# Kernel tuning notes

Measured on AMD Instinct MI355X. Metric: run time of the kernel, lower is better.

Reference implementation:

```python
import jax, jax.numpy as jnp
import numpy as np

B, L, C, V = 16, 600, 256, 256
OUT_SEQ = 6000
KSZ = 5
DILATIONS = (1, 2, 4)
N_BLOCKS = 10
COND = 256  # speaker(128) + noise(128)
TEMP = 10.0
EPS = 1e-5


def _ccbn(x, cond, gw, gb, bw, bb):
    # x: (B, C, L); conditional batch-norm: per-channel stats over (batch, length),
    # gamma/beta predicted from condition vector.
    mu = jnp.mean(x, axis=(0, 2), keepdims=True)
    var = jnp.var(x, axis=(0, 2), keepdims=True)
    xn = (x - mu) * jax.lax.rsqrt(var + EPS)
    gamma = 1.0 + cond @ gw + gb  # (B, C)
    beta = cond @ bw + bb         # (B, C)
    return xn * gamma[:, :, None] + beta[:, :, None]


def _conv1d(x, w, b, dil=1):
    # x: (B, C_in, L); w: (C_out, C_in, K)
    y = jax.lax.conv_general_dilated(
        x, w, window_strides=(1,), padding='SAME', rhs_dilation=(dil,),
        dimension_numbers=('NCH', 'OIH', 'NCH'))
    return y + b[None, :, None]


def setup_inputs() -> dict:
    key = jax.random.key(0)
    ks = jax.random.split(key, 20)
    s = 0.02
    inp = {
        'inputs': jax.random.randint(ks[0], (B, L), 0, V),
        'speaker_embeddings': jax.random.normal(ks[1], (B, 128), jnp.float32),
        'noise': jax.random.normal(ks[2], (B, 128), jnp.float32),
        'emb': jax.random.normal(ks[3], (V, C), jnp.float32) * s,
        # 10 blocks x 3 dilated convs
        'conv_w': jax.random.normal(ks[4], (N_BLOCKS, 3, C, C, KSZ), jnp.float32) * s,
        'conv_b': jnp.zeros((N_BLOCKS, 3, C), jnp.float32),
        # CCBN projections per conv (gamma/beta from condition)
        'g_w': jax.random.normal(ks[5], (N_BLOCKS, 3, COND, C), jnp.float32) * s,
        'g_b': jnp.zeros((N_BLOCKS, 3, C), jnp.float32),
        'b_w': jax.random.normal(ks[6], (N_BLOCKS, 3, COND, C), jnp.float32) * s,
        'b_b': jnp.zeros((N_BLOCKS, 3, C), jnp.float32),
        # TokenLength head: 2 CCBNs + conv1 (256->256,k1) + conv2 (256->1,k1)
        'tl_g_w': jax.random.normal(ks[7], (2, COND, C), jnp.float32) * s,
        'tl_g_b': jnp.zeros((2, C), jnp.float32),
        'tl_b_w': jax.random.normal(ks[8], (2, COND, C), jnp.float32) * s,
        'tl_b_b': jnp.zeros((2, C), jnp.float32),
        'tl_conv1_w': jax.random.normal(ks[9], (C, C, 1), jnp.float32) * s,
        'tl_conv1_b': jnp.zeros((C,), jnp.float32),
        'tl_conv2_w': jax.random.normal(ks[10], (1, C, 1), jnp.float32) * s,
        'tl_conv2_b': jnp.zeros((1,), jnp.float32),
    }
    return inp


def reference(inputs, speaker_embeddings, noise, emb, conv_w, conv_b,
              g_w, g_b, b_w, b_b, tl_g_w, tl_g_b, tl_b_w, tl_b_b,
              tl_conv1_w, tl_conv1_b, tl_conv2_w, tl_conv2_b):
    cond = jnp.concatenate([speaker_embeddings, noise], axis=-1)  # (B, COND)
    x = emb[inputs]                    # (B, L, C)
    x = jnp.transpose(x, (0, 2, 1))    # (B, C, L)

    # 10 unaligned blocks: residual stacks of CCBN -> ReLU -> dilated conv
    for blk in range(N_BLOCKS):
        y = x
        for j, d in enumerate(DILATIONS):
            y = jax.nn.relu(_ccbn(y, cond, g_w[blk, j], g_b[blk, j], b_w[blk, j], b_b[blk, j]))
            y = _conv1d(y, conv_w[blk, j], conv_b[blk, j], dil=d)
        x = x + y
    unaligned = x  # (B, C, L)

    # TokenLength head
    t = jax.nn.relu(_ccbn(unaligned, cond, tl_g_w[0], tl_g_b[0], tl_b_w[0], tl_b_b[0]))
    t = _conv1d(t, tl_conv1_w, tl_conv1_b)
    t = jax.nn.relu(_ccbn(t, cond, tl_g_w[1], tl_g_b[1], tl_b_w[1], tl_b_b[1]))
    t = _conv1d(t, tl_conv2_w, tl_conv2_b)  # (B, 1, L)
    token_lengths = jax.nn.relu(t[:, 0, :])  # (B, L)

    token_ends = jnp.cumsum(token_lengths, axis=-1)        # (B, L)
    token_centers = token_ends - token_lengths / 2.0        # (B, L)
    aligned_lengths = token_ends

    out_pos = jnp.arange(OUT_SEQ, dtype=jnp.float32)         # (OUT,)
    diff = token_centers[:, None, :] - out_pos[None, :, None]  # (B, OUT, L)
    logits = -(diff * diff) / TEMP
    weights = jax.nn.softmax(logits, axis=-1)                # (B, OUT, L)

    feats = jnp.transpose(unaligned, (0, 2, 1))              # (B, L, C)
    aligned_features = jnp.einsum('bol,blc->boc', weights, feats)  # (B, OUT, C)
    return aligned_features, aligned_lengths
```

## Files before the change

kernel.cpp:

```cpp
#include <hip/hip_runtime.h>
#include <math.h>

#define EPSv 1e-5f

typedef short short8 __attribute__((ext_vector_type(8)));
typedef float floatx4 __attribute__((ext_vector_type(4)));

__device__ __forceinline__ unsigned short f2bf(float x) {
  unsigned u = __float_as_uint(x);
  unsigned r = (u + 0x7fffu + ((u >> 16) & 1u)) >> 16;
  return (unsigned short)r;
}

__global__ void k_zero(float* __restrict__ p) {
  p[blockIdx.x * 256 + threadIdx.x] = 0.f;
}

__global__ void k_gamma_beta(const float* __restrict__ spk, const float* __restrict__ noise,
                             const float* __restrict__ g_w, const float* __restrict__ g_b,
                             const float* __restrict__ b_w, const float* __restrict__ b_b,
                             const float* __restrict__ tl_g_w, const float* __restrict__ tl_g_b,
                             const float* __restrict__ tl_b_w, const float* __restrict__ tl_b_b,
                             float* __restrict__ gammas, float* __restrict__ betas) {
  __shared__ float condl[16*256];
  int t = threadIdx.x;
  for (int idx = t; idx < 4096; idx += 256) {
    int b = idx >> 8, k = idx & 255;
    condl[idx] = (k < 128) ? spk[b*128 + k] : noise[b*128 + k - 128];
  }
  __syncthreads();
  int i = blockIdx.x;
  const float *gw, *bw, *gbias, *bbias;
  if (i < 30) { gw = g_w + (size_t)i*65536; bw = b_w + (size_t)i*65536; gbias = g_b + i*256; bbias = b_b + i*256; }
  else { int j = i - 30; gw = tl_g_w + (size_t)j*65536; bw = tl_b_w + (size_t)j*65536; gbias = tl_g_b + j*256; bbias = tl_b_b + j*256; }
  int co = (t & 63) + blockIdx.y * 64;
  int slot = t >> 6;
  float g[4] = {0.f,0.f,0.f,0.f}, bt[4] = {0.f,0.f,0.f,0.f};
  for (int k = 0; k < 256; ++k) {
    float gwv = gw[k*256 + co];
    float bwv = bw[k*256 + co];
    #pragma unroll
    for (int bb = 0; bb < 4; ++bb) {
      float cv = condl[(slot*4 + bb)*256 + k];
      g[bb]  = fmaf(cv, gwv, g[bb]);
      bt[bb] = fmaf(cv, bwv, bt[bb]);
    }
  }
  #pragma unroll
  for (int bb = 0; bb < 4; ++bb) {
    int b = slot*4 + bb;
    gammas[i*4096 + b*256 + co] = 1.0f + g[bb] + gbias[co];
    betas [i*4096 + b*256 + co] = bt[bb] + bbias[co];
  }
}

template<int TAPS>
__device__ __forceinline__ void wprep_body(const float* __restrict__ src,
                                           unsigned short* __restrict__ dst,
                                           int cotile, int chunk, int t) {
  int cow = t >> 2, ci8 = (t & 3) * 8;
  const float* s0 = src + ((size_t)(cotile*64 + cow)*256 + chunk*32 + ci8)*TAPS;
  float v[8*TAPS];
  #pragma unroll
  for (int i = 0; i < 8*TAPS; ++i) v[i] = s0[i];
  unsigned short* dblk = dst + (size_t)cotile*(8*TAPS*4096) + (size_t)chunk*(TAPS*4096);
  #pragma unroll
  for (int tap = 0; tap < TAPS; ++tap) {
    unsigned hi2[4], lo2[4];
    #pragma unroll
    for (int jj = 0; jj < 4; ++jj) {
      float a = v[(jj*2+0)*TAPS + tap], b = v[(jj*2+1)*TAPS + tap];
      unsigned short ha = f2bf(a), hb = f2bf(b);
      unsigned short la = f2bf(a - __uint_as_float((unsigned)ha << 16));
      unsigned short lb = f2bf(b - __uint_as_float((unsigned)hb << 16));
      hi2[jj] = (unsigned)ha | ((unsigned)hb << 16);
      lo2[jj] = (unsigned)la | ((unsigned)lb << 16);
    }
    uint4 H; H.x = hi2[0]; H.y = hi2[1]; H.z = hi2[2]; H.w = hi2[3];
    uint4 L; L.x = lo2[0]; L.y = lo2[1]; L.z = lo2[2]; L.w = lo2[3];
    *(uint4*)(dblk + (size_t)(tap*2)*2048 + cow*32 + ci8) = H;
    *(uint4*)(dblk + (size_t)(tap*2+1)*2048 + cow*32 + ci8) = L;
  }
}

__global__ __launch_bounds__(256) void k_wprep(const float* __restrict__ conv_w,
                                               const float* __restrict__ tl_c1_w,
                                               unsigned short* __restrict__ wp) {
  int cc = blockIdx.x;
  int cotile = blockIdx.y >> 3, chunk = blockIdx.y & 7;
  if (cc == 30) wprep_body<1>(tl_c1_w, wp + (size_t)30*655360, cotile, chunk, threadIdx.x);
  else          wprep_body<5>(conv_w + (size_t)cc*327680, wp + (size_t)cc*655360, cotile, chunk, threadIdx.x);
}

__global__ void k_embed2(const int* __restrict__ inp, const float* __restrict__ emb,
                         float* __restrict__ x, float* __restrict__ stat0) {
  int bx = blockIdx.x;
  int c = threadIdx.x;
  int r0 = bx * 60;
  float s = 0.f, s2 = 0.f;
  for (int r = 0; r < 60; ++r) {
    int row = inp[r0 + r];
    float v = emb[(size_t)row*256 + c];
    x[(size_t)(r0 + r)*256 + c] = v;
    s += v; s2 = fmaf(v, v, s2);
  }
  atomicAdd(&stat0[c], s);
  atomicAdd(&stat0[256 + c], s2);
}

template<int TAPS>
__global__ __launch_bounds__(256) void k_convm(const float* __restrict__ zin, float* __restrict__ out,
                        const float* __restrict__ stat_in, float* __restrict__ stat_out,
                        const float* __restrict__ gam, const float* __restrict__ bet,
                        const unsigned short* __restrict__ wpc,
                        const float* __restrict__ bias, int dil, int mode) {
  __shared__ unsigned short Zhi[3200];
  __shared__ unsigned short Zlo[3200];
  __shared__ float s_sc[256];
  __shared__ float s_sh[256];
  __shared__ float lsum[32];
  __shared__ float lsq[32];
  int t = threadIdx.x;
  int bx = blockIdx.x;
  int b  = bx / 10;
  int l0 = (bx % 10) * 64;
  int co0 = blockIdx.y * 32;
  int cobase = (blockIdx.y & 1) * 32;
  int PAD = ((TAPS - 1)/2) * dil;
  int ROWS = 64 + 2*PAD;
  int w = t >> 6, lane = t & 63;
  int lsub = (w & 1) * 32, cosub = (w >> 1) * 16;
  int quad = lane >> 4, nlan = lane & 15;
  if (t < 32) { lsum[t] = 0.f; lsq[t] = 0.f; }
  {
    float s = stat_in[t], s2 = stat_in[256 + t];
    float mu = s * (1.0f/9600.0f);
    float var = s2 * (1.0f/9600.0f) - mu*mu;
    float rs = rsqrtf(var + EPSv);
    float scale = rs * gam[b*256 + t];
    s_sc[t] = scale;
    s_sh[t] = fmaf(-mu, scale, bet[b*256 + t]);
  }

  floatx4 acc[2];
  acc[0] = (floatx4){0.f,0.f,0.f,0.f};
  acc[1] = (floatx4){0.f,0.f,0.f,0.f};

  const float* zb = zin + (size_t)b*600*256;
  int srow = t >> 3, fq = t & 7;
  int ar0 = (lsub + nlan) * 40 + quad * 8;
  int ar1 = (lsub + 16 + nlan) * 40 + quad * 8;

  bool va[3]; long zbase[3];
  #pragma unroll
  for (int i = 0; i < 3; ++i) {
    int r = srow + i*32;
    int gl = l0 - PAD + r;
    va[i] = (r < ROWS) && (gl >= 0) && (gl < 600);
    zbase[i] = (long)gl*256 + fq*4;
  }

  for (int chunk = 0; chunk < 8; ++chunk) {
    int ci0 = chunk * 32;
    const unsigned short* pch = wpc + (size_t)((blockIdx.y >> 1)*8 + chunk) * (TAPS*4096);
    short8 bh[TAPS], bl[TAPS];
    int cw = (cobase + cosub + nlan)*32 + quad*8;
    #pragma unroll
    for (int tap = 0; tap < TAPS; ++tap) {
      bh[tap] = *(const short8*)(pch + (size_t)(tap*2)*2048 + cw);
      bl[tap] = *(const short8*)(pch + (size_t)(tap*2+1)*2048 + cw);
    }
    float4 zr[3];
    #pragma unroll
    for (int i = 0; i < 3; ++i) {
      float4 z = {0.f,0.f,0.f,0.f};
      if (va[i]) z = *(const float4*)&zb[zbase[i] + ci0];
      zr[i] = z;
    }
    __syncthreads();
    float4 sc4 = *(const float4*)&s_sc[ci0 + fq*4];
    float4 sh4 = *(const float4*)&s_sh[ci0 + fq*4];
    #pragma unroll
    for (int i = 0; i < 3; ++i) {
      int r = srow + i*32;
      if (r < ROWS) {
        float4 z = zr[i];
        bool inr = va[i];
        float v0 = inr ? fmaxf(fmaf(z.x, sc4.x, sh4.x), 0.f) : 0.f;
        float v1 = inr ? fmaxf(fmaf(z.y, sc4.y, sh4.y), 0.f) : 0.f;
        float v2 = inr ? fmaxf(fmaf(z.z, sc4.z, sh4.z), 0.f) : 0.f;
        float v3 = inr ? fmaxf(fmaf(z.w, sc4.w, sh4.w), 0.f) : 0.f;
        unsigned short h0 = f2bf(v0), h1 = f2bf(v1), h2 = f2bf(v2), h3 = f2bf(v3);
        unsigned short e0 = f2bf(v0 - __uint_as_float((unsigned)h0 << 16));
        unsigned short e1 = f2bf(v1 - __uint_as_float((unsigned)h1 << 16));
        unsigned short e2 = f2bf(v2 - __uint_as_float((unsigned)h2 << 16));
        unsigned short e3 = f2bf(v3 - __uint_as_float((unsigned)h3 << 16));
        uint2 vh; vh.x = (unsigned)h0 | ((unsigned)h1 << 16);
        vh.y = (unsigned)h2 | ((unsigned)h3 << 16);
        uint2 vl; vl.x = (unsigned)e0 | ((unsigned)e1 << 16);
        vl.y = (unsigned)e2 | ((unsigned)e3 << 16);
        *(uint2*)&Zhi[r*40 + fq*4] = vh;
        *(uint2*)&Zlo[r*40 + fq*4] = vl;
      }
    }
    __syncthreads();
    #pragma unroll
    for (int tap = 0; tap < TAPS; ++tap) {
      int sh = tap * dil * 40;
      short8 ah0 = *(const short8*)&Zhi[ar0 + sh];
      short8 ah1 = *(const short8*)&Zhi[ar1 + sh];
      short8 al0 = *(const short8*)&Zlo[ar0 + sh];
      short8 al1 = *(const short8*)&Zlo[ar1 + sh];
      acc[0] = __builtin_amdgcn_mfma_f32_16x16x32_bf16(ah0, bh[tap], acc[0], 0, 0, 0);
      acc[0] = __builtin_amdgcn_mfma_f32_16x16x32_bf16(ah0, bl[tap], acc[0], 0, 0, 0);
      acc[0] = __builtin_amdgcn_mfma_f32_16x16x32_bf16(al0, bh[tap], acc[0], 0, 0, 0);
      acc[1] = __builtin_amdgcn_mfma_f32_16x16x32_bf16(ah1, bh[tap], acc[1], 0, 0, 0);
      acc[1] = __builtin_amdgcn_mfma_f32_16x16x32_bf16(ah1, bl[tap], acc[1], 0, 0, 0);
      acc[1] = __builtin_amdgcn_mfma_f32_16x16x32_bf16(al1, bh[tap], acc[1], 0, 0, 0);
    }
  }

  float bsv = bias[co0 + cosub + nlan];
  float ssum = 0.f, ssq = 0.f;
  #pragma unroll
  for (int mt = 0; mt < 2; ++mt) {
    #pragma unroll
    for (int r = 0; r < 4; ++r) {
      int l = l0 + lsub + mt*16 + quad*4 + r;
      if (l < 600) {
        float v = acc[mt][r] + bsv;
        float* dst = &out[((size_t)(b*600 + l))*256 + co0 + cosub + nlan];
        if (mode) v += *dst;
        *dst = v;
        ssum += v;
        ssq = fmaf(v, v, ssq);
      }
    }
  }
  ssum += __shfl_xor(ssum, 16, 64);
  ssum += __shfl_xor(ssum, 32, 64);
  ssq  += __shfl_xor(ssq, 16, 64);
  ssq  += __shfl_xor(ssq, 32, 64);
  if (quad == 0) {
    atomicAdd(&lsum[cosub + nlan], ssum);
    atomicAdd(&lsq [cosub + nlan], ssq);
  }
  __syncthreads();
  if (t < 32) {
    atomicAdd(&stat_out[co0 + t], lsum[t]);
    atomicAdd(&stat_out[256 + co0 + t], lsq[t]);
  }
}

__global__ void k_tl2(const float* __restrict__ z, const float* __restrict__ stat,
                      const float* __restrict__ gam, const float* __restrict__ bet,
                      const float* __restrict__ w2, const float* __restrict__ b2,
                      float* __restrict__ tl) {
  int t = threadIdx.x;
  int row = blockIdx.x * 4 + (t >> 6);
  int lane = t & 63;
  int b = row / 600;
  float4 s1 = *(const float4*)&stat[lane*4];
  float4 s2 = *(const float4*)&stat[256 + lane*4];
  float4 gm = *(const float4*)&gam[b*256 + lane*4];
  float4 bt = *(const float4*)&bet[b*256 + lane*4];
  float sc[4], sh[4];
  {
    float sv[4] = {s1.x, s1.y, s1.z, s1.w};
    float qv[4] = {s2.x, s2.y, s2.z, s2.w};
    float gv[4] = {gm.x, gm.y, gm.z, gm.w};
    float bv[4] = {bt.x, bt.y, bt.z, bt.w};
    #pragma unroll
    for (int i = 0; i < 4; ++i) {
      float mu = sv[i] * (1.0f/9600.0f);
      float var = qv[i] * (1.0f/9600.0f) - mu*mu;
      float rs = rsqrtf(var + EPSv);
      sc[i] = rs * gv[i];
      sh[i] = fmaf(-mu, sc[i], bv[i]);
    }
  }
  float4 zr = *(const float4*)&z[(size_t)row*256 + lane*4];
  float4 wr = *(const float4*)&w2[lane*4];
  float z0 = fmaxf(fmaf(zr.x, sc[0], sh[0]), 0.f);
  float z1 = fmaxf(fmaf(zr.y, sc[1], sh[1]), 0.f);
  float z2 = fmaxf(fmaf(zr.z, sc[2], sh[2]), 0.f);
  float z3 = fmaxf(fmaf(zr.w, sc[3], sh[3]), 0.f);
  float s = z0*wr.x + z1*wr.y + z2*wr.z + z3*wr.w;
  for (int m = 32; m >= 1; m >>= 1) s += __shfl_xor(s, m, 64);
  if (lane == 0) tl[row] = fmaxf(s + b2[0], 0.f);
}

__global__ void k_cumsum(const float* __restrict__ tl, float* __restrict__ centers,
                         float* __restrict__ out_len) {
  int b = blockIdx.x; int lane = threadIdx.x;
  float carry = 0.f;
  for (int ch = 0; ch < 10; ++ch) {
    int l = ch*64 + lane;
    float v = (l < 600) ? tl[b*600 + l] : 0.f;
    float s = v;
    #pragma unroll
    for (int off = 1; off < 64; off <<= 1) {
      float n = __shfl_up(s, off, 64);
      if (lane >= off) s += n;
    }
    float ends = carry + s;
    if (l < 600) {
      centers[b*600 + l] = ends - 0.5f*v;
      out_len[b*600 + l] = ends;
    }
    carry = __shfl(ends, 63, 64);
  }
}

__global__ void k_tobf16(const float* __restrict__ x, unsigned short* __restrict__ fbT) {
  __shared__ unsigned short T[64*66];
  int b = blockIdx.x, lt = blockIdx.y, ct = blockIdx.z;
  int t = threadIdx.x;
  int i4 = t >> 6;
  int j = t & 63;
  #pragma unroll
  for (int r = 0; r < 16; ++r) {
    int li = i4*16 + r;
    int l = lt*64 + li;
    float v = (l < 600) ? x[((size_t)(b*600 + l))*256 + ct*64 + j] : 0.f;
    T[j*66 + li] = f2bf(v);
  }
  __syncthreads();
  int row = t >> 2, seg = (t & 3) * 16;
  unsigned vv[8];
  #pragma unroll
  for (int k = 0; k < 8; ++k)
    vv[k] = *(const unsigned*)&T[row*66 + seg + k*2];
  size_t dsth = ((size_t)(b*256 + ct*64 + row))*640 + lt*64 + seg;
  unsigned* du = (unsigned*)fbT;
  uint4 a; a.x = vv[0]; a.y = vv[1]; a.z = vv[2]; a.w = vv[3];
  uint4 c4; c4.x = vv[4]; c4.y = vv[5]; c4.z = vv[6]; c4.w = vv[7];
  *(uint4*)(du + dsth/2) = a;
  *(uint4*)(du + dsth/2 + 4) = c4;
}

__global__ __launch_bounds__(256) void k_align2(const unsigned short* __restrict__ fbT,
                        const float* __restrict__ centers, float* __restrict__ outp) {
  __shared__ float cen[600];
  __shared__ float mrow[64];
  __shared__ float isum[64];
  __shared__ unsigned short Wt[64*72];
  __shared__ unsigned short Ft[256*72];
  int b = blockIdx.x;
  int o0 = blockIdx.y * 64;
  int t = threadIdx.x;
  int wv = t >> 6, lane = t & 63;
  for (int i = t; i < 600; i += 256) cen[i] = centers[b*600 + i];
  __syncthreads();
  for (int rr = 0; rr < 16; ++rr) {
    int oi = wv*16 + rr;
    float opos = (float)(o0 + oi);
    float mx = -3.0e38f;
    for (int l = lane; l < 600; l += 64) {
      float d = cen[l] - opos;
      mx = fmaxf(mx, -d*d*0.1f);
    }
    #pragma unroll
    for (int mm = 32; mm >= 1; mm >>= 1) mx = fmaxf(mx, __shfl_xor(mx, mm, 64));
    if (lane == 0) mrow[oi] = mx;
  }
  __syncthreads();
  floatx4 acc[4][4];
  #pragma unroll
  for (int i = 0; i < 4; ++i)
    #pragma unroll
    for (int j = 0; j < 4; ++j)
      acc[i][j] = (floatx4){0.f, 0.f, 0.f, 0.f};
  int quad = lane >> 4;
  int nlan = lane & 15;
  int oi_w = t >> 2;
  int sbase = t & 3;
  float mo = mrow[oi_w];
  float opos_w = (float)(o0 + oi_w);
  float psum = 0.f;
  const unsigned short* srcb = fbT + ((size_t)b*256)*640;

  for (int ch = 0; ch < 10; ++ch) {
    int lc0 = ch * 64;
    __syncthreads();
    #pragma unroll
    for (int sidx = 0; sidx < 2; ++sidx) {
      int seg = sbase + sidx*4;
      unsigned pk[4];
      #pragma unroll
      for (int jj = 0; jj < 8; jj += 2) {
        int li = lc0 + seg*8 + jj;
        float e0 = 0.f, e1 = 0.f;
        if (li < 600)     { float d = cen[li] - opos_w;     e0 = __expf(-d*d*0.1f - mo); }
        if (li + 1 < 600) { float d = cen[li + 1] - opos_w; e1 = __expf(-d*d*0.1f - mo); }
        psum += e0 + e1;
        pk[jj>>1] = (unsigned)f2bf(e0) | ((unsigned)f2bf(e1) << 16);
      }
      uint4 v; v.x = pk[0]; v.y = pk[1]; v.z = pk[2]; v.w = pk[3];
      *(uint4*)&Wt[oi_w*72 + seg*8] = v;
    }
    #pragma unroll
    for (int it = 0; it < 8; ++it) {
      int idx = t + it*256;
      int c = idx >> 3, part = idx & 7;
      uint4 v = *(const uint4*)(srcb + (size_t)c*640 + lc0 + part*8);
      *(uint4*)&Ft[c*72 + part*8] = v;
    }
    __syncthreads();
    #pragma unroll
    for (int ks = 0; ks < 2; ++ks) {
      int ko = ks*32 + quad*8;
      short8 af[4], bfr[4];
      #pragma unroll
      for (int mt = 0; mt < 4; ++mt)
        af[mt] = *(const short8*)&Wt[(mt*16 + nlan)*72 + ko];
      #pragma unroll
      for (int nt = 0; nt < 4; ++nt)
        bfr[nt] = *(const short8*)&Ft[(wv*64 + nt*16 + nlan)*72 + ko];
      #pragma unroll
      for (int mt = 0; mt < 4; ++mt)
        #pragma unroll
        for (int nt = 0; nt < 4; ++nt)
          acc[mt][nt] = __builtin_amdgcn_mfma_f32_16x16x32_bf16(af[mt], bfr[nt], acc[mt][nt], 0, 0, 0);
    }
  }
  psum += __shfl_xor(psum, 1, 64);
  psum += __shfl_xor(psum, 2, 64);
  if ((t & 3) == 0) isum[oi_w] = 1.0f / psum;
  __syncthreads();
  #pragma unroll
  for (int mt = 0; mt < 4; ++mt) {
    #pragma unroll
    for (int r = 0; r < 4; ++r) {
      int oi = mt*16 + quad*4 + r;
      int o = o0 + oi;
      if (o < 6000) {
        float sc = isum[oi];
        #pragma unroll
        for (int nt = 0; nt < 4; ++nt) {
          int c = wv*64 + nt*16 + nlan;
          outp[((size_t)b*6000 + o)*256 + c] = acc[mt][nt][r] * sc;
        }
      }
    }
  }
}

extern "C" void kernel_launch(void* const* d_in, const int* in_sizes, int n_in,
                              void* d_out, int out_size, void* d_ws, size_t ws_size,
                              hipStream_t stream) {
  const int*   inputs = (const int*)  d_in[0];
  const float* spk    = (const float*)d_in[1];
  const float* noise  = (const float*)d_in[2];
  const float* emb    = (const float*)d_in[3];
  const float* conv_w = (const float*)d_in[4];
  const float* conv_b = (const float*)d_in[5];
  const float* g_w    = (const float*)d_in[6];
  const float* g_b    = (const float*)d_in[7];
  const float* b_w    = (const float*)d_in[8];
  const float* b_b    = (const float*)d_in[9];
  const float* tl_g_w = (const float*)d_in[10];
  const float* tl_g_b = (const float*)d_in[11];
  const float* tl_b_w = (const float*)d_in[12];
  const float* tl_b_b = (const float*)d_in[13];
  const float* tl_c1_w = (const float*)d_in[14];
  const float* tl_c1_b = (const float*)d_in[15];
  const float* tl_c2_w = (const float*)d_in[16];
  const float* tl_c2_b = (const float*)d_in[17];
  float* out = (float*)d_out;

  float* ws = (float*)d_ws;
  float* x       = ws;
  float* A       = x + 2457600;
  float* Bf      = A + 2457600;
  float* gammas  = Bf + 2457600;
  float* betas   = gammas + 131072;
  float* statacc = betas + 131072;
  float* tl      = statacc + 16384;
  float* cen     = tl + 9600;
  unsigned short* wp = (unsigned short*)(cen + 9600);
  unsigned short* fbT = (unsigned short*)Bf;

  k_zero<<<dim3(64), dim3(256), 0, stream>>>(statacc);
  k_wprep<<<dim3(31, 32), dim3(256), 0, stream>>>(conv_w, tl_c1_w, wp);
  k_gamma_beta<<<dim3(32, 4), dim3(256), 0, stream>>>(spk, noise, g_w, g_b, b_w, b_b,
      tl_g_w, tl_g_b, tl_b_w, tl_b_b, gammas, betas);
  k_embed2<<<dim3(160), dim3(256), 0, stream>>>(inputs, emb, x, statacc);

  const int dils[3] = {1, 2, 4};
  for (int blk = 0; blk < 10; ++blk) {
    const float* srcs[3] = {x, A, Bf};
    float*       dsts[3] = {A, Bf, x};
    for (int j = 0; j < 3; ++j) {
      int idx = blk*3 + j;
      int mode = (j == 2) ? 1 : 0;
      k_convm<5><<<dim3(160, 8), dim3(256), 0, stream>>>(srcs[j], dsts[j],
          statacc + idx*512, statacc + (idx+1)*512,
          gammas + idx*4096, betas + idx*4096,
          wp + (size_t)idx*655360, conv_b + idx*256, dils[j], mode);
    }
  }
  k_convm<1><<<dim3(160, 8), dim3(256), 0, stream>>>(x, A,
      statacc + 30*512, statacc + 31*512,
      gammas + 30*4096, betas + 30*4096,
      wp + (size_t)30*655360, tl_c1_b, 1, 0);
  k_tl2<<<dim3(2400), dim3(256), 0, stream>>>(A, statacc + 31*512,
      gammas + 31*4096, betas + 31*4096, tl_c2_w, tl_c2_b, tl);
  k_cumsum<<<dim3(16), dim3(64), 0, stream>>>(tl, cen, out + 24576000);
  k_tobf16<<<dim3(16, 10, 4), dim3(256), 0, stream>>>(x, fbT);
  k_align2<<<dim3(16, 94), dim3(256), 0, stream>>>(fbT, cen, out);
}
```

Before: 1.662 ms.

## Precompute normalized bf16 hi/lo activations in separate kernel, load via direct-to-LDS

Moves the conditional batch-norm, ReLU and bf16 hi/lo split out of the conv kernel into a new k_norm kernel. It writes padded, chunked bf16 tiles to a workspace once per layer, so the transform is no longer repeated by all 8 output-channel blocks. The conv kernel then fills its shared-memory tiles with global_load_lds DMA transfers instead of register loads plus ALU conversion. In exchange it adds an extra kernel launch per layer and a global round trip of the normalized tensor.

```diff
diff --git a/kernel.cpp b/kernel.cpp
--- a/kernel.cpp
+++ b/kernel.cpp
@@ -1,5 +1,6 @@
 #include <hip/hip_runtime.h>
 #include <math.h>
+#include <stdint.h>
 
 #define EPSv 1e-5f
 
@@ -10,6 +11,13 @@
   unsigned u = __float_as_uint(x);
   unsigned r = (u + 0x7fffu + ((u >> 16) & 1u)) >> 16;
   return (unsigned short)r;
+}
+
+__device__ __forceinline__ void gld_lds16(const void* g, void* l) {
+  __builtin_amdgcn_global_load_lds(
+      (const __attribute__((address_space(1))) unsigned*)(uintptr_t)g,
+      (__attribute__((address_space(3))) unsigned*)(uintptr_t)l,
+      16, 0, 0);
 }
 
 __global__ void k_zero(float* __restrict__ p) {
@@ -108,16 +116,67 @@
   atomicAdd(&stat0[256 + c], s2);
 }
 
+__global__ __launch_bounds__(256) void k_norm(const float* __restrict__ z,
+                      const float* __restrict__ stat,
+                      const float* __restrict__ gam, const float* __restrict__ bet,
+                      unsigned short* __restrict__ zn) {
+  __shared__ float s_sc[32];
+  __shared__ float s_sh[32];
+  int b = blockIdx.x, chunk = blockIdx.y, rg = blockIdx.z;
+  int t = threadIdx.x;
+  if (t < 32) {
+    int c = chunk*32 + t;
+    float s = stat[c], s2 = stat[256 + c];
+    float mu = s * (1.0f/9600.0f);
+    float var = s2 * (1.0f/9600.0f) - mu*mu;
+    float rs = rsqrtf(var + EPSv);
+    float scale = rs * gam[b*256 + c];
+    s_sc[t] = scale;
+    s_sh[t] = fmaf(-mu, scale, bet[b*256 + c]);
+  }
+  __syncthreads();
+  int srow = t >> 3, fq = t & 7;
+  float4 sc4 = *(const float4*)&s_sc[fq*4];
+  float4 sh4 = *(const float4*)&s_sh[fq*4];
+  unsigned short* zh = zn + ((size_t)b*8 + chunk)*54400 + fq*4;
+  unsigned short* zl = zh + 27200;
+  const float* zb = z + (size_t)b*600*256 + chunk*32 + fq*4;
+  #pragma unroll
+  for (int i = 0; i < 4; ++i) {
+    int r = rg*128 + i*32 + srow;
+    if (r < 680) {
+      int l = r - 8;
+      uint2 vh; vh.x = 0u; vh.y = 0u;
+      uint2 vl; vl.x = 0u; vl.y = 0u;
+      if (l >= 0 && l < 600) {
+        float4 zv = *(const float4*)&zb[(size_t)l*256];
+        float v0 = fmaxf(fmaf(zv.x, sc4.x, sh4.x), 0.f);
+        float v1 = fmaxf(fmaf(zv.y, sc4.y, sh4.y), 0.f);
+        float v2 = fmaxf(fmaf(zv.z, sc4.z, sh4.z), 0.f);
+        float v3 = fmaxf(fmaf(zv.w, sc4.w, sh4.w), 0.f);
+        unsigned short h0 = f2bf(v0), h1 = f2bf(v1), h2 = f2bf(v2), h3 = f2bf(v3);
+        unsigned short e0 = f2bf(v0 - __uint_as_float((unsigned)h0 << 16));
+        unsigned short e1 = f2bf(v1 - __uint_as_float((unsigned)h1 << 16));
+        unsigned short e2 = f2bf(v2 - __uint_as_float((unsigned)h2 << 16));
+        unsigned short e3 = f2bf(v3 - __uint_as_float((unsigned)h3 << 16));
+        vh.x = (unsigned)h0 | ((unsigned)h1 << 16);
+        vh.y = (unsigned)h2 | ((unsigned)h3 << 16);
+        vl.x = (unsigned)e0 | ((unsigned)e1 << 16);
+        vl.y = (unsigned)e2 | ((unsigned)e3 << 16);
+      }
+      *(uint2*)&zh[(size_t)r*40] = vh;
+      *(uint2*)&zl[(size_t)r*40] = vl;
+    }
+  }
+}
+
 template<int TAPS>
-__global__ __launch_bounds__(256) void k_convm(const float* __restrict__ zin, float* __restrict__ out,
-                        const float* __restrict__ stat_in, float* __restrict__ stat_out,
-                        const float* __restrict__ gam, const float* __restrict__ bet,
+__global__ __launch_bounds__(256) void k_convm(const unsigned short* __restrict__ zn,
+                        float* __restrict__ out, float* __restrict__ stat_out,
                         const unsigned short* __restrict__ wpc,
                         const float* __restrict__ bias, int dil, int mode) {
-  __shared__ unsigned short Zhi[3200];
-  __shared__ unsigned short Zlo[3200];
-  __shared__ float s_sc[256];
-  __shared__ float s_sh[256];
+  __shared__ __align__(16) unsigned short Zhi[3584];
+  __shared__ __align__(16) unsigned short Zlo[3584];
   __shared__ float lsum[32];
   __shared__ float lsq[32];
   int t = threadIdx.x;
@@ -127,41 +186,21 @@
   int co0 = blockIdx.y * 32;
   int cobase = (blockIdx.y & 1) * 32;
   int PAD = ((TAPS - 1)/2) * dil;
-  int ROWS = 64 + 2*PAD;
   int w = t >> 6, lane = t & 63;
   int lsub = (w & 1) * 32, cosub = (w >> 1) * 16;
   int quad = lane >> 4, nlan = lane & 15;
   if (t < 32) { lsum[t] = 0.f; lsq[t] = 0.f; }
-  {
-    float s = stat_in[t], s2 = stat_in[256 + t];
-    float mu = s * (1.0f/9600.0f);
-    float var = s2 * (1.0f/9600.0f) - mu*mu;
-    float rs = rsqrtf(var + EPSv);
-    float scale = rs * gam[b*256 + t];
-    s_sc[t] = scale;
-    s_sh[t] = fmaf(-mu, scale, bet[b*256 + t]);
-  }
 
   floatx4 acc[2];
   acc[0] = (floatx4){0.f,0.f,0.f,0.f};
   acc[1] = (floatx4){0.f,0.f,0.f,0.f};
 
-  const float* zb = zin + (size_t)b*600*256;
-  int srow = t >> 3, fq = t & 7;
+  const unsigned short* zbase = zn + (size_t)b*435200 + (size_t)(l0 - PAD + 8)*40 + (size_t)lane*8;
   int ar0 = (lsub + nlan) * 40 + quad * 8;
-  int ar1 = (lsub + 16 + nlan) * 40 + quad * 8;
-
-  bool va[3]; long zbase[3];
-  #pragma unroll
-  for (int i = 0; i < 3; ++i) {
-    int r = srow + i*32;
-    int gl = l0 - PAD + r;
-    va[i] = (r < ROWS) && (gl >= 0) && (gl < 600);
-    zbase[i] = (long)gl*256 + fq*4;
-  }
+  int ar1 = ar0 + 640;
 
   for (int chunk = 0; chunk < 8; ++chunk) {
-    int ci0 = chunk * 32;
+    __syncthreads();
     const unsigned short* pch = wpc + (size_t)((blockIdx.y >> 1)*8 + chunk) * (TAPS*4096);
     short8 bh[TAPS], bl[TAPS];
     int cw = (cobase + cosub + nlan)*32 + quad*8;
@@ -170,38 +209,13 @@
       bh[tap] = *(const short8*)(pch + (size_t)(tap*2)*2048 + cw);
       bl[tap] = *(const short8*)(pch + (size_t)(tap*2+1)*2048 + cw);
     }
-    float4 zr[3];
-    #pragma unroll
-    for (int i = 0; i < 3; ++i) {
-      float4 z = {0.f,0.f,0.f,0.f};
-      if (va[i]) z = *(const float4*)&zb[zbase[i] + ci0];
-      zr[i] = z;
-    }
-    __syncthreads();
-    float4 sc4 = *(const float4*)&s_sc[ci0 + fq*4];
-    float4 sh4 = *(const float4*)&s_sh[ci0 + fq*4];
-    #pragma unroll
-    for (int i = 0; i < 3; ++i) {
-      int r = srow + i*32;
-      if (r < ROWS) {
-        float4 z = zr[i];
-        bool inr = va[i];
-        float v0 = inr ? fmaxf(fmaf(z.x, sc4.x, sh4.x), 0.f) : 0.f;
-        float v1 = inr ? fmaxf(fmaf(z.y, sc4.y, sh4.y), 0.f) : 0.f;
-        float v2 = inr ? fmaxf(fmaf(z.z, sc4.z, sh4.z), 0.f) : 0.f;
-        float v3 = inr ? fmaxf(fmaf(z.w, sc4.w, sh4.w), 0.f) : 0.f;
-        unsigned short h0 = f2bf(v0), h1 = f2bf(v1), h2 = f2bf(v2), h3 = f2bf(v3);
-        unsigned short e0 = f2bf(v0 - __uint_as_float((unsigned)h0 << 16));
-        unsigned short e1 = f2bf(v1 - __uint_as_float((unsigned)h1 << 16));
-        unsigned short e2 = f2bf(v2 - __uint_as_float((unsigned)h2 << 16));
-        unsigned short e3 = f2bf(v3 - __uint_as_float((unsigned)h3 << 16));
-        uint2 vh; vh.x = (unsigned)h0 | ((unsigned)h1 << 16);
-        vh.y = (unsigned)h2 | ((unsigned)h3 << 16);
-        uint2 vl; vl.x = (unsigned)e0 | ((unsigned)e1 << 16);
-        vl.y = (unsigned)e2 | ((unsigned)e3 << 16);
-        *(uint2*)&Zhi[r*40 + fq*4] = vh;
-        *(uint2*)&Zlo[r*40 + fq*4] = vl;
-      }
+    const unsigned short* srcp = zbase + (size_t)chunk*54400;
+    for (int i = w; i < 14; i += 4) {
+      int p = (i >= 7) ? 1 : 0;
+      int k = i - p*7;
+      const unsigned short* g = srcp + p*27200 + k*512;
+      unsigned short* lp = (p ? Zlo : Zhi) + k*512;
+      gld_lds16(g, lp);
     }
     __syncthreads();
     #pragma unroll
@@ -479,6 +493,7 @@
   float* tl      = statacc + 16384;
   float* cen     = tl + 9600;
   unsigned short* wp = (unsigned short*)(cen + 9600);
+  unsigned short* Zn = wp + (size_t)31*655360;
   unsigned short* fbT = (unsigned short*)Bf;
 
   k_zero<<<dim3(64), dim3(256), 0, stream>>>(statacc);
@@ -494,15 +509,17 @@
     for (int j = 0; j < 3; ++j) {
       int idx = blk*3 + j;
       int mode = (j == 2) ? 1 : 0;
-      k_convm<5><<<dim3(160, 8), dim3(256), 0, stream>>>(srcs[j], dsts[j],
-          statacc + idx*512, statacc + (idx+1)*512,
-          gammas + idx*4096, betas + idx*4096,
+      k_norm<<<dim3(16, 8, 6), dim3(256), 0, stream>>>(srcs[j],
+          statacc + idx*512, gammas + idx*4096, betas + idx*4096, Zn);
+      k_convm<5><<<dim3(160, 8), dim3(256), 0, stream>>>(Zn, dsts[j],
+          statacc + (idx+1)*512,
           wp + (size_t)idx*655360, conv_b + idx*256, dils[j], mode);
     }
   }
-  k_convm<1><<<dim3(160, 8), dim3(256), 0, stream>>>(x, A,
-      statacc + 30*512, statacc + 31*512,
-      gammas + 30*4096, betas + 30*4096,
+  k_norm<<<dim3(16, 8, 6), dim3(256), 0, stream>>>(x,
+      statacc + 30*512, gammas + 30*4096, betas + 30*4096, Zn);
+  k_convm<1><<<dim3(160, 8), dim3(256), 0, stream>>>(Zn, A,
+      statacc + 31*512,
       wp + (size_t)30*655360, tl_c1_b, 1, 0);
   k_tl2<<<dim3(2400), dim3(256), 0, stream>>>(A, statacc + 31*512,
       gammas + 31*4096, betas + 31*4096, tl_c2_w, tl_c2_b, tl);
```

New measurement: 1.692 ms. Within noise of the previous version (+1.8%).
